# Performance work log

Hardware: AMD Instinct MI355X
Metric: run time of the kernel (lower is better)

The kernel has to match this reference:

```python
import jax, jax.numpy as jnp
import numpy as np
from functools import partial

POOL_LIST = (1, 2, 4)   # SPP pyramid: 1 + 4 + 16 = 21 bins per channel
NUM_ROIS = 256
H = 64
W = 64
C = 512


def setup_inputs() -> dict:
    key = jax.random.key(0)
    k1, k2, k3 = jax.random.split(key, 3)
    img = jax.random.normal(k1, (1, H, W, C), dtype=jnp.float32)
    # rois = (x, y, w, h) in feature-map pixels; chosen so every bin is
    # non-empty and in-bounds (x+h <= W, y+w <= H given the code's axis swap).
    xy = jax.random.uniform(k2, (1, NUM_ROIS, 2), jnp.float32, 0.0, 32.0)
    wh = jax.random.uniform(k3, (1, NUM_ROIS, 2), jnp.float32, 8.0, 31.0)
    rois = jnp.concatenate([xy, wh], axis=-1)
    return {"img": img, "rois": rois}


@partial(jax.jit, static_argnames=("pool_list",))
def _roi_pool(img, rois, pool_list):
    feat = img[0]                     # (H, W, C), channels_last
    Hf, Wf, Cc = feat.shape
    R = rois.shape[1]
    x = rois[0, :, 0]
    y = rois[0, :, 1]
    w = rois[0, :, 2]
    h = rois[0, :, 3]
    wi = jnp.arange(Wf)
    hi = jnp.arange(Hf)
    NEG = jnp.asarray(-jnp.inf, feat.dtype)
    outs = []
    for p in pool_list:               # small static pyramid loop
        # Faithful to original: x-axis bin length uses h/p (col_length),
        # y-axis bin length uses w/p (row_length).
        col_len = h / p               # (R,) for x direction
        row_len = w / p               # (R,) for y direction
        idx = jnp.arange(p, dtype=rois.dtype)
        # bin boundaries, round-half-to-even like tf.round / K.round
        x1 = jnp.round(x[:, None] + idx * col_len[:, None]).astype(jnp.int32)        # (R, p)
        x2 = jnp.round(x[:, None] + (idx + 1.0) * col_len[:, None]).astype(jnp.int32)
        y1 = jnp.round(y[:, None] + idx * row_len[:, None]).astype(jnp.int32)
        y2 = jnp.round(y[:, None] + (idx + 1.0) * row_len[:, None]).astype(jnp.int32)
        mx = (wi >= x1[..., None]) & (wi < x2[..., None])   # (R, p, W)
        my = (hi >= y1[..., None]) & (hi < y2[..., None])   # (R, p, H)
        # masked max over W per (roi, x-bin): fused select+reduce under jit
        colmax = jnp.max(jnp.where(mx[:, :, None, :, None], feat[None, None], NEG), axis=3)  # (R, p, H, C)
        # masked max over H per (roi, x-bin, y-bin)
        binmax = jnp.max(jnp.where(my[:, None, :, :, None], colmax[:, :, None, :, :], NEG), axis=3)  # (R, p_ix, p_jy, C)
        # original loop order: ix outer, jy inner, channels fastest
        outs.append(binmax.reshape(R, p * p, Cc))
    out = jnp.concatenate(outs, axis=1)   # (R, sum(p*p), C)
    return out.reshape(1, R, -1)          # (1, num_rois, C * 21)


def reference(img, rois):
    return _roi_pool(img, rois, POOL_LIST)
```

## Files before the change

kernel.cpp:

```cpp
#include <hip/hip_runtime.h>
#include <math.h>

#define HF 64
#define WF 64
#define CC 512
#define NROI 256
#define NBINS 21

__device__ __forceinline__ float4 max4(float4 a, float4 b) {
    float4 r;
    r.x = fmaxf(a.x, b.x); r.y = fmaxf(a.y, b.y);
    r.z = fmaxf(a.z, b.z); r.w = fmaxf(a.w, b.w);
    return r;
}

__global__ __launch_bounds__(256) void roi_pool_fused(
    const float* __restrict__ img,
    const float* __restrict__ rois,
    float* __restrict__ out)
{
    __shared__ float fineLds[4][4][64];
    __shared__ float p2Lds[2][2][64];

    const int bid  = blockIdx.x;
    const int e    = bid & 7;
    const int roi  = bid >> 3;
    const int tid  = threadIdx.x;
    const int wv   = tid >> 6;
    const int lane = tid & 63;
    const int pp   = lane >> 4;
    const int cl   = lane & 15;
    const int c0   = e * 64 + cl * 4;

    const float x = rois[roi * 4 + 0];
    const float y = rois[roi * 4 + 1];
    const float w = rois[roi * 4 + 2];
    const float h = rois[roi * 4 + 3];

    const float clh = h * 0.25f;
    const float clw = w * 0.25f;

    int bx[5];
#pragma unroll
    for (int i = 0; i < 5; ++i)
        bx[i] = (int)rintf(__fadd_rn(x, __fmul_rn((float)i, clh)));

    const int y1 = (int)rintf(__fadd_rn(y, __fmul_rn((float)wv,       clw)));
    const int y2 = (int)rintf(__fadd_rn(y, __fmul_rn((float)(wv + 1), clw)));

    float4 acc[4];
#pragma unroll
    for (int jx = 0; jx < 4; ++jx) {
        acc[jx].x = -INFINITY; acc[jx].y = -INFINITY;
        acc[jx].z = -INFINITY; acc[jx].w = -INFINITY;
    }

    const float* base = img + c0;
    for (int hh = y1; hh < y2; ++hh) {
        const float* rowp = base + (size_t)hh * (WF * CC);
#pragma unroll
        for (int jx = 0; jx < 4; ++jx) {
            for (int ww = bx[jx] + pp; ww < bx[jx + 1]; ww += 4) {
                acc[jx] = max4(acc[jx], *(const float4*)(rowp + (size_t)ww * CC));
            }
        }
    }

#pragma unroll
    for (int jx = 0; jx < 4; ++jx) {
        float4 a = acc[jx];
        a.x = fmaxf(a.x, __shfl_xor(a.x, 16));
        a.y = fmaxf(a.y, __shfl_xor(a.y, 16));
        a.z = fmaxf(a.z, __shfl_xor(a.z, 16));
        a.w = fmaxf(a.w, __shfl_xor(a.w, 16));
        a.x = fmaxf(a.x, __shfl_xor(a.x, 32));
        a.y = fmaxf(a.y, __shfl_xor(a.y, 32));
        a.z = fmaxf(a.z, __shfl_xor(a.z, 32));
        a.w = fmaxf(a.w, __shfl_xor(a.w, 32));
        acc[jx] = a;
    }

    float* outr = out + (size_t)roi * (NBINS * CC) + c0;

    if (lane < 16) {
#pragma unroll
        for (int jx = 0; jx < 4; ++jx) {
            *(float4*)(outr + (size_t)(5 + jx * 4 + wv) * CC) = acc[jx];
            *(float4*)(&fineLds[wv][jx][cl * 4]) = acc[jx];
        }
    }
    __syncthreads();

    {
        const int i2 = wv >> 1;
        const int j2 = wv & 1;
        if (lane < 16) {
            const float4 f00 = *(const float4*)(&fineLds[2*j2  ][2*i2  ][cl * 4]);
            const float4 f01 = *(const float4*)(&fineLds[2*j2  ][2*i2+1][cl * 4]);
            const float4 f10 = *(const float4*)(&fineLds[2*j2+1][2*i2  ][cl * 4]);
            const float4 f11 = *(const float4*)(&fineLds[2*j2+1][2*i2+1][cl * 4]);
            const float4 a = max4(max4(f00, f01), max4(f10, f11));
            *(float4*)(outr + (size_t)(1 + i2 * 2 + j2) * CC) = a;
            *(float4*)(&p2Lds[i2][j2][cl * 4]) = a;
        }
    }
    __syncthreads();

    if (wv == 0 && lane < 16) {
        const float4 a00 = *(const float4*)(&p2Lds[0][0][cl * 4]);
        const float4 a01 = *(const float4*)(&p2Lds[0][1][cl * 4]);
        const float4 a10 = *(const float4*)(&p2Lds[1][0][cl * 4]);
        const float4 a11 = *(const float4*)(&p2Lds[1][1][cl * 4]);
        *(float4*)(outr) = max4(max4(a00, a01), max4(a10, a11));
    }
}

extern "C" void kernel_launch(void* const* d_in, const int* in_sizes, int n_in,
                              void* d_out, int out_size, void* d_ws, size_t ws_size,
                              hipStream_t stream) {
    const float* img  = (const float*)d_in[0];
    const float* rois = (const float*)d_in[1];
    float* out = (float*)d_out;

    dim3 grid(NROI * 8);
    dim3 block(256);
    roi_pool_fused<<<grid, block, 0, stream>>>(img, rois, out);
}
```

Before: 25.67 us.

## Assign one wave per fine bin with 1024-thread blocks and 128-channel slices

Restructures the work split so each 1024-thread block handles a 128-channel slice of one ROI. Each of its 16 waves owns one (jy, jx) fine bin, and the two wave halves stride over W. The inner loop processes two rows at once with separate accumulators to expose more memory-level parallelism. The grid is reordered so adjacent blocks take adjacent ROIs. This removes the serial loop over four x-bins per wave and reduces the shuffle reduction, at the cost of larger blocks and fewer of them, which may reduce occupancy flexibility and add per-bin imbalance.

```diff
diff --git a/kernel.cpp b/kernel.cpp
--- a/kernel.cpp
+++ b/kernel.cpp
@@ -14,23 +14,25 @@
     return r;
 }
 
-__global__ __launch_bounds__(256) void roi_pool_fused(
+__global__ __launch_bounds__(1024) void roi_pool_fused(
     const float* __restrict__ img,
     const float* __restrict__ rois,
     float* __restrict__ out)
 {
-    __shared__ float fineLds[4][4][64];
-    __shared__ float p2Lds[2][2][64];
+    __shared__ float fineLds[4][4][128];
+    __shared__ float p2Lds[2][2][128];
 
     const int bid  = blockIdx.x;
-    const int e    = bid & 7;
-    const int roi  = bid >> 3;
+    const int q    = (bid & 7) >> 1;
+    const int roi  = ((bid >> 3) << 1) | (bid & 1);
     const int tid  = threadIdx.x;
     const int wv   = tid >> 6;
+    const int jy   = wv >> 2;
+    const int jx   = wv & 3;
     const int lane = tid & 63;
-    const int pp   = lane >> 4;
-    const int cl   = lane & 15;
-    const int c0   = e * 64 + cl * 4;
+    const int half = lane >> 5;
+    const int cl   = lane & 31;
+    const int c0   = q * 128 + cl * 4;
 
     const float x = rois[roi * 4 + 0];
     const float y = rois[roi * 4 + 1];
@@ -40,73 +42,68 @@
     const float clh = h * 0.25f;
     const float clw = w * 0.25f;
 
-    int bx[5];
-#pragma unroll
-    for (int i = 0; i < 5; ++i)
-        bx[i] = (int)rintf(__fadd_rn(x, __fmul_rn((float)i, clh)));
+    const int x1 = (int)rintf(__fadd_rn(x, __fmul_rn((float)jx,       clh)));
+    const int x2 = (int)rintf(__fadd_rn(x, __fmul_rn((float)(jx + 1), clh)));
+    const int y1 = (int)rintf(__fadd_rn(y, __fmul_rn((float)jy,       clw)));
+    const int y2 = (int)rintf(__fadd_rn(y, __fmul_rn((float)(jy + 1), clw)));
 
-    const int y1 = (int)rintf(__fadd_rn(y, __fmul_rn((float)wv,       clw)));
-    const int y2 = (int)rintf(__fadd_rn(y, __fmul_rn((float)(wv + 1), clw)));
-
-    float4 acc[4];
-#pragma unroll
-    for (int jx = 0; jx < 4; ++jx) {
-        acc[jx].x = -INFINITY; acc[jx].y = -INFINITY;
-        acc[jx].z = -INFINITY; acc[jx].w = -INFINITY;
-    }
+    float4 accA, accB;
+    accA.x = -INFINITY; accA.y = -INFINITY; accA.z = -INFINITY; accA.w = -INFINITY;
+    accB = accA;
 
     const float* base = img + c0;
-    for (int hh = y1; hh < y2; ++hh) {
-        const float* rowp = base + (size_t)hh * (WF * CC);
-#pragma unroll
-        for (int jx = 0; jx < 4; ++jx) {
-            for (int ww = bx[jx] + pp; ww < bx[jx + 1]; ww += 4) {
-                acc[jx] = max4(acc[jx], *(const float4*)(rowp + (size_t)ww * CC));
+    int hh = y1;
+    for (; hh + 1 < y2; hh += 2) {
+        const float* r0 = base + (size_t)hh * (WF * CC);
+        const float* r1 = r0 + (WF * CC);
+        for (int ww0 = x1; ww0 < x2; ww0 += 2) {
+            const int ww = ww0 + half;
+            if (ww < x2) {
+                const float4 v0 = *(const float4*)(r0 + (size_t)ww * CC);
+                const float4 v1 = *(const float4*)(r1 + (size_t)ww * CC);
+                accA = max4(accA, v0);
+                accB = max4(accB, v1);
             }
         }
     }
+    if (hh < y2) {
+        const float* r0 = base + (size_t)hh * (WF * CC);
+        for (int ww0 = x1; ww0 < x2; ww0 += 2) {
+            const int ww = ww0 + half;
+            if (ww < x2) {
+                accA = max4(accA, *(const float4*)(r0 + (size_t)ww * CC));
+            }
+        }
+    }
+    float4 acc = max4(accA, accB);
 
-#pragma unroll
-    for (int jx = 0; jx < 4; ++jx) {
-        float4 a = acc[jx];
-        a.x = fmaxf(a.x, __shfl_xor(a.x, 16));
-        a.y = fmaxf(a.y, __shfl_xor(a.y, 16));
-        a.z = fmaxf(a.z, __shfl_xor(a.z, 16));
-        a.w = fmaxf(a.w, __shfl_xor(a.w, 16));
-        a.x = fmaxf(a.x, __shfl_xor(a.x, 32));
-        a.y = fmaxf(a.y, __shfl_xor(a.y, 32));
-        a.z = fmaxf(a.z, __shfl_xor(a.z, 32));
-        a.w = fmaxf(a.w, __shfl_xor(a.w, 32));
-        acc[jx] = a;
-    }
+    acc.x = fmaxf(acc.x, __shfl_xor(acc.x, 32));
+    acc.y = fmaxf(acc.y, __shfl_xor(acc.y, 32));
+    acc.z = fmaxf(acc.z, __shfl_xor(acc.z, 32));
+    acc.w = fmaxf(acc.w, __shfl_xor(acc.w, 32));
 
     float* outr = out + (size_t)roi * (NBINS * CC) + c0;
 
-    if (lane < 16) {
-#pragma unroll
-        for (int jx = 0; jx < 4; ++jx) {
-            *(float4*)(outr + (size_t)(5 + jx * 4 + wv) * CC) = acc[jx];
-            *(float4*)(&fineLds[wv][jx][cl * 4]) = acc[jx];
-        }
+    if (half == 0) {
+        *(float4*)(outr + (size_t)(5 + jx * 4 + jy) * CC) = acc;
+        *(float4*)(&fineLds[jy][jx][cl * 4]) = acc;
     }
     __syncthreads();
 
-    {
+    if (wv < 4 && half == 0) {
         const int i2 = wv >> 1;
         const int j2 = wv & 1;
-        if (lane < 16) {
-            const float4 f00 = *(const float4*)(&fineLds[2*j2  ][2*i2  ][cl * 4]);
-            const float4 f01 = *(const float4*)(&fineLds[2*j2  ][2*i2+1][cl * 4]);
-            const float4 f10 = *(const float4*)(&fineLds[2*j2+1][2*i2  ][cl * 4]);
-            const float4 f11 = *(const float4*)(&fineLds[2*j2+1][2*i2+1][cl * 4]);
-            const float4 a = max4(max4(f00, f01), max4(f10, f11));
-            *(float4*)(outr + (size_t)(1 + i2 * 2 + j2) * CC) = a;
-            *(float4*)(&p2Lds[i2][j2][cl * 4]) = a;
-        }
+        const float4 f00 = *(const float4*)(&fineLds[2*j2  ][2*i2  ][cl * 4]);
+        const float4 f01 = *(const float4*)(&fineLds[2*j2  ][2*i2+1][cl * 4]);
+        const float4 f10 = *(const float4*)(&fineLds[2*j2+1][2*i2  ][cl * 4]);
+        const float4 f11 = *(const float4*)(&fineLds[2*j2+1][2*i2+1][cl * 4]);
+        const float4 a = max4(max4(f00, f01), max4(f10, f11));
+        *(float4*)(outr + (size_t)(1 + i2 * 2 + j2) * CC) = a;
+        *(float4*)(&p2Lds[i2][j2][cl * 4]) = a;
     }
     __syncthreads();
 
-    if (wv == 0 && lane < 16) {
+    if (wv == 0 && half == 0) {
         const float4 a00 = *(const float4*)(&p2Lds[0][0][cl * 4]);
         const float4 a01 = *(const float4*)(&p2Lds[0][1][cl * 4]);
         const float4 a10 = *(const float4*)(&p2Lds[1][0][cl * 4]);
@@ -122,7 +119,7 @@
     const float* rois = (const float*)d_in[1];
     float* out = (float*)d_out;
 
-    dim3 grid(NROI * 8);
-    dim3 block(256);
+    dim3 grid(NROI * 4);
+    dim3 block(1024);
     roi_pool_fused<<<grid, block, 0, stream>>>(img, rois, out);
 }
```

Result: faster. 21.20 us (-17.4%).

## Restructure ROI pooling work split: 128-channel tiles, row-split waves, clamped uniform column loop

Applied to the files above, without the earlier changes.

Each block now handles 128 channels with 512 threads. Pairs of waves split the rows of each y-bin, and each half-wave takes alternate columns. The four x-bins are walked in one uniform loop of length K, with column indices clamped, so the variable-trip inner loops are replaced by unrolled loads that can be issued together. Addressing uses 32-bit byte offsets. The cost is redundant clamped reloads for narrower bins and an extra LDS stage to merge the two row halves.

```diff
diff --git a/kernel.cpp b/kernel.cpp
--- a/kernel.cpp
+++ b/kernel.cpp
@@ -1,5 +1,6 @@
 #include <hip/hip_runtime.h>
 #include <math.h>
+#include <stdint.h>
 
 #define HF 64
 #define WF 64
@@ -14,23 +15,30 @@
     return r;
 }
 
-__global__ __launch_bounds__(256) void roi_pool_fused(
+__device__ __forceinline__ float4 ld4(const float* __restrict__ img, uint32_t byteoff) {
+    return *(const float4*)((const char*)img + byteoff);
+}
+
+__global__ __launch_bounds__(512, 8) void roi_pool_fused(
     const float* __restrict__ img,
     const float* __restrict__ rois,
     float* __restrict__ out)
 {
-    __shared__ float fineLds[4][4][64];
-    __shared__ float p2Lds[2][2][64];
+    __shared__ float ldsA[4][2][4][128];
+    __shared__ float ldsB[4][4][128];
+    __shared__ float ldsC[2][2][128];
 
     const int bid  = blockIdx.x;
-    const int e    = bid & 7;
-    const int roi  = bid >> 3;
+    const int q    = (bid & 7) >> 1;
+    const int roi  = ((bid >> 3) << 1) | (bid & 1);
     const int tid  = threadIdx.x;
     const int wv   = tid >> 6;
+    const int jy   = wv >> 1;
+    const int rp   = wv & 1;
     const int lane = tid & 63;
-    const int pp   = lane >> 4;
-    const int cl   = lane & 15;
-    const int c0   = e * 64 + cl * 4;
+    const int half = lane >> 5;
+    const int cl   = lane & 31;
+    const int c0   = q * 128 + cl * 4;
 
     const float x = rois[roi * 4 + 0];
     const float y = rois[roi * 4 + 1];
@@ -45,8 +53,12 @@
     for (int i = 0; i < 5; ++i)
         bx[i] = (int)rintf(__fadd_rn(x, __fmul_rn((float)i, clh)));
 
-    const int y1 = (int)rintf(__fadd_rn(y, __fmul_rn((float)wv,       clw)));
-    const int y2 = (int)rintf(__fadd_rn(y, __fmul_rn((float)(wv + 1), clw)));
+    const int y1 = (int)rintf(__fadd_rn(y, __fmul_rn((float)jy,       clw)));
+    const int y2 = (int)rintf(__fadd_rn(y, __fmul_rn((float)(jy + 1), clw)));
+
+    const int w01 = max(bx[1] - bx[0], bx[2] - bx[1]);
+    const int w23 = max(bx[3] - bx[2], bx[4] - bx[3]);
+    const int K   = (max(w01, w23) + 1) >> 1;
 
     float4 acc[4];
 #pragma unroll
@@ -55,13 +67,18 @@
         acc[jx].z = -INFINITY; acc[jx].w = -INFINITY;
     }
 
-    const float* base = img + c0;
-    for (int hh = y1; hh < y2; ++hh) {
-        const float* rowp = base + (size_t)hh * (WF * CC);
+    const uint32_t ROWB = WF * CC * 4;
+    const uint32_t PXB  = CC * 4;
+    const uint32_t cb   = (uint32_t)c0 * 4;
+
+    for (int r = y1 + rp; r < y2; r += 2) {
+        const uint32_t ro = cb + (uint32_t)r * ROWB;
+        for (int k = 0; k < K; ++k) {
+            const int cc2 = 2 * k + half;
 #pragma unroll
-        for (int jx = 0; jx < 4; ++jx) {
-            for (int ww = bx[jx] + pp; ww < bx[jx + 1]; ww += 4) {
-                acc[jx] = max4(acc[jx], *(const float4*)(rowp + (size_t)ww * CC));
+            for (int jx = 0; jx < 4; ++jx) {
+                const int col = min(bx[jx] + cc2, bx[jx + 1] - 1);
+                acc[jx] = max4(acc[jx], ld4(img, ro + (uint32_t)col * PXB));
             }
         }
     }
@@ -69,10 +86,6 @@
 #pragma unroll
     for (int jx = 0; jx < 4; ++jx) {
         float4 a = acc[jx];
-        a.x = fmaxf(a.x, __shfl_xor(a.x, 16));
-        a.y = fmaxf(a.y, __shfl_xor(a.y, 16));
-        a.z = fmaxf(a.z, __shfl_xor(a.z, 16));
-        a.w = fmaxf(a.w, __shfl_xor(a.w, 16));
         a.x = fmaxf(a.x, __shfl_xor(a.x, 32));
         a.y = fmaxf(a.y, __shfl_xor(a.y, 32));
         a.z = fmaxf(a.z, __shfl_xor(a.z, 32));
@@ -80,37 +93,44 @@
         acc[jx] = a;
     }
 
+    if (half == 0) {
+#pragma unroll
+        for (int jx = 0; jx < 4; ++jx)
+            *(float4*)(&ldsA[jy][rp][jx][cl * 4]) = acc[jx];
+    }
+    __syncthreads();
+
     float* outr = out + (size_t)roi * (NBINS * CC) + c0;
 
-    if (lane < 16) {
+    if (rp == 0 && half == 0) {
 #pragma unroll
         for (int jx = 0; jx < 4; ++jx) {
-            *(float4*)(outr + (size_t)(5 + jx * 4 + wv) * CC) = acc[jx];
-            *(float4*)(&fineLds[wv][jx][cl * 4]) = acc[jx];
+            const float4 m = max4(*(const float4*)(&ldsA[jy][0][jx][cl * 4]),
+                                  *(const float4*)(&ldsA[jy][1][jx][cl * 4]));
+            *(float4*)(outr + (size_t)(5 + jx * 4 + jy) * CC) = m;
+            *(float4*)(&ldsB[jy][jx][cl * 4]) = m;
         }
     }
     __syncthreads();
 
-    {
+    if (wv < 4 && half == 0) {
         const int i2 = wv >> 1;
         const int j2 = wv & 1;
-        if (lane < 16) {
-            const float4 f00 = *(const float4*)(&fineLds[2*j2  ][2*i2  ][cl * 4]);
-            const float4 f01 = *(const float4*)(&fineLds[2*j2  ][2*i2+1][cl * 4]);
-            const float4 f10 = *(const float4*)(&fineLds[2*j2+1][2*i2  ][cl * 4]);
-            const float4 f11 = *(const float4*)(&fineLds[2*j2+1][2*i2+1][cl * 4]);
-            const float4 a = max4(max4(f00, f01), max4(f10, f11));
-            *(float4*)(outr + (size_t)(1 + i2 * 2 + j2) * CC) = a;
-            *(float4*)(&p2Lds[i2][j2][cl * 4]) = a;
-        }
+        const float4 f00 = *(const float4*)(&ldsB[2*j2  ][2*i2  ][cl * 4]);
+        const float4 f01 = *(const float4*)(&ldsB[2*j2  ][2*i2+1][cl * 4]);
+        const float4 f10 = *(const float4*)(&ldsB[2*j2+1][2*i2  ][cl * 4]);
+        const float4 f11 = *(const float4*)(&ldsB[2*j2+1][2*i2+1][cl * 4]);
+        const float4 a = max4(max4(f00, f01), max4(f10, f11));
+        *(float4*)(outr + (size_t)(1 + i2 * 2 + j2) * CC) = a;
+        *(float4*)(&ldsC[i2][j2][cl * 4]) = a;
     }
     __syncthreads();
 
-    if (wv == 0 && lane < 16) {
-        const float4 a00 = *(const float4*)(&p2Lds[0][0][cl * 4]);
-        const float4 a01 = *(const float4*)(&p2Lds[0][1][cl * 4]);
-        const float4 a10 = *(const float4*)(&p2Lds[1][0][cl * 4]);
-        const float4 a11 = *(const float4*)(&p2Lds[1][1][cl * 4]);
+    if (wv == 0 && half == 0) {
+        const float4 a00 = *(const float4*)(&ldsC[0][0][cl * 4]);
+        const float4 a01 = *(const float4*)(&ldsC[0][1][cl * 4]);
+        const float4 a10 = *(const float4*)(&ldsC[1][0][cl * 4]);
+        const float4 a11 = *(const float4*)(&ldsC[1][1][cl * 4]);
         *(float4*)(outr) = max4(max4(a00, a01), max4(a10, a11));
     }
 }
@@ -122,7 +142,7 @@
     const float* rois = (const float*)d_in[1];
     float* out = (float*)d_out;
 
-    dim3 grid(NROI * 8);
-    dim3 block(256);
+    dim3 grid(NROI * 4);
+    dim3 block(512);
     roi_pool_fused<<<grid, block, 0, stream>>>(img, rois, out);
 }
```

New measurement: 21.55 us. 1.19x faster.
